# Optimization experiments

Hardware: AMD Instinct MI355X
Metric: run time of the kernel (lower is better)

The kernel has to match this reference:

```python
import jax, jax.numpy as jnp
import numpy as np

EMBED = 1024
N_HEADS = 16
HEAD_DIM = EMBED // N_HEADS
B, T = 2, 2048


def setup_inputs() -> dict:
    key = jax.random.key(0)
    k1, k2, k3 = jax.random.split(key, 3)
    x = jax.random.normal(k1, (B, T, EMBED), dtype=jnp.float32)
    # torch nn.Linear(embed, 3*embed, bias=False): weight [3C, C]; store as [C, 3C] for x @ W
    w_attn = jax.random.normal(k2, (EMBED, 3 * EMBED), dtype=jnp.float32) * (EMBED ** -0.5)
    w_proj = jax.random.normal(k3, (EMBED, EMBED), dtype=jnp.float32) * (EMBED ** -0.5)
    return {"x": x, "w_attn": w_attn, "w_proj": w_proj}


def reference(x, w_attn, w_proj):
    Bb, Tt, C = x.shape
    kqv = x @ w_attn  # [B, T, 3C]
    # NOTE: original code unpacks as k, q, v (k first)
    k, q, v = jnp.split(kqv, 3, axis=2)
    def heads(t):
        return t.reshape(Bb, Tt, N_HEADS, HEAD_DIM).transpose(0, 2, 1, 3)  # [B, H, T, D]
    k, q, v = heads(k), heads(q), heads(v)
    scale = HEAD_DIM ** -0.5
    wei = jnp.einsum("bhqd,bhkd->bhqk", q, k) * scale  # [B, H, T, T]
    mask = jnp.tril(jnp.ones((Tt, Tt), dtype=bool))
    wei = jnp.where(mask[None, None], wei, -jnp.inf)
    wei = jax.nn.softmax(wei, axis=-1)
    y = jnp.einsum("bhqk,bhkd->bhqd", wei, v)  # [B, H, T, D]
    y = y.transpose(0, 2, 1, 3).reshape(Bb, Tt, C)
    return y @ w_proj
```

## Files before the change

kernel.cpp:

```cpp
#include <hip/hip_runtime.h>

typedef unsigned short u16;
typedef unsigned int u32;

typedef __attribute__((ext_vector_type(4))) float f32x4;
typedef __attribute__((ext_vector_type(8))) short s16x8;
typedef __attribute__((ext_vector_type(4))) short s16x4;

__device__ __forceinline__ u16 f2bf(float f) {
    u32 u = __builtin_bit_cast(u32, f);
    u += 0x7fffu + ((u >> 16) & 1u);
    return (u16)(u >> 16);
}

__device__ __forceinline__ u32 pk_bf16(float a, float b) {
    return (u32)f2bf(a) | ((u32)f2bf(b) << 16);
}

__device__ __forceinline__ u32 cvtpk(float a, float b) {
    u32 r;
    asm("v_cvt_pk_bf16_f32 %0, %1, %2" : "=v"(r) : "v"(a), "v"(b));
    return r;
}

#define EXP2(x) exp2f(x)

__device__ __forceinline__ void gload16(const u16* g, u16* l) {
    __builtin_amdgcn_global_load_lds(
        (const __attribute__((address_space(1))) void*)(const void*)g,
        (__attribute__((address_space(3))) void*)(void*)l, 16, 0, 0);
}

__global__ void k_cast(const float* __restrict__ in, u16* __restrict__ out) {
    int i = (blockIdx.x * 256 + threadIdx.x) * 4;
    float4 v = *(const float4*)(in + i);
    uint2 pk;
    pk.x = pk_bf16(v.x, v.y);
    pk.y = pk_bf16(v.z, v.w);
    *(uint2*)(out + i) = pk;
}

__global__ void k_transpose(const float* __restrict__ in, u16* __restrict__ out,
                            int K, int N) {
    __shared__ float tile[32][33];
    int n0 = blockIdx.x * 32, k0 = blockIdx.y * 32;
    int x = threadIdx.x, y = threadIdx.y;
#pragma unroll
    for (int j = 0; j < 32; j += 8)
        tile[y + j][x] = in[(size_t)(k0 + y + j) * N + n0 + x];
    __syncthreads();
#pragma unroll
    for (int j = 0; j < 32; j += 8)
        out[(size_t)(n0 + y + j) * K + k0 + x] = f2bf(tile[x][y + j]);
}

template <int EPI>
__global__ __launch_bounds__(256, 2) void k_gemm(
        const u16* __restrict__ A, const u16* __restrict__ Bt,
        void* __restrict__ Cout, u16* __restrict__ Vt, int N, int K) {
    __shared__ u16 As[128 * 32];
    __shared__ u16 Bs[128 * 32];
    const int nbn = N >> 7;
    const int bm = (int)blockIdx.x / nbn, bn = (int)blockIdx.x % nbn;
    const int tid = threadIdx.x;
    const int wv = tid >> 6, ln = tid & 63;
    const int lg = ln >> 4, lr = ln & 15;
    const int wr = (wv >> 1) << 6, wc = (wv & 1) << 6;

    const u16* gA = A + (size_t)(bm * 128 + wv * 32 + (ln >> 2)) * K + (ln & 3) * 8;
    const u16* gB = Bt + (size_t)(bn * 128 + wv * 32 + (ln >> 2)) * K + (ln & 3) * 8;
    u16* lA = As + wv * 1024;
    u16* lB = Bs + wv * 1024;

    f32x4 acc[4][4] = {};

    for (int k0 = 0; k0 < K; k0 += 32) {
        gload16(gA + k0, lA);
        gload16(gA + k0 + 16 * K, lA + 512);
        gload16(gB + k0, lB);
        gload16(gB + k0 + 16 * K, lB + 512);
        __syncthreads();
        s16x8 af[4], bf[4];
#pragma unroll
        for (int mi = 0; mi < 4; ++mi)
            af[mi] = *(const s16x8*)&As[(wr + mi * 16 + lr) * 32 + lg * 8];
#pragma unroll
        for (int ni = 0; ni < 4; ++ni)
            bf[ni] = *(const s16x8*)&Bs[(wc + ni * 16 + lr) * 32 + lg * 8];
#pragma unroll
        for (int mi = 0; mi < 4; ++mi)
#pragma unroll
            for (int ni = 0; ni < 4; ++ni)
                acc[mi][ni] = __builtin_amdgcn_mfma_f32_16x16x32_bf16(
                        af[mi], bf[ni], acc[mi][ni], 0, 0, 0);
        __syncthreads();
    }

    const int crow0 = bm * 128 + wr + lg * 4;
    const int ccol0 = bn * 128 + wc + lr;
    if (EPI == 0) {
        float* Co = (float*)Cout;
#pragma unroll
        for (int mi = 0; mi < 4; ++mi)
#pragma unroll
            for (int ni = 0; ni < 4; ++ni)
#pragma unroll
                for (int r = 0; r < 4; ++r)
                    Co[(size_t)(crow0 + mi * 16 + r) * N + ccol0 + ni * 16] =
                            acc[mi][ni][r];
    } else {
        if (bn < 16) {
            const float qs = (bn >= 8) ? 0.18033688011112042f : 1.0f;
            u16* Co = (u16*)Cout;
#pragma unroll
            for (int mi = 0; mi < 4; ++mi)
#pragma unroll
                for (int ni = 0; ni < 4; ++ni)
#pragma unroll
                    for (int r = 0; r < 4; ++r)
                        Co[(size_t)(crow0 + mi * 16 + r) * 3072 + ccol0 + ni * 16] =
                                f2bf(acc[mi][ni][r] * qs);
        } else {
#pragma unroll
            for (int mi = 0; mi < 4; ++mi) {
                int row = crow0 + mi * 16;
                int bb = row >> 11, t = row & 2047;
#pragma unroll
                for (int ni = 0; ni < 4; ++ni) {
                    int hd = ccol0 + ni * 16 - 2048;
                    uint2 pk;
                    pk.x = pk_bf16(acc[mi][ni][0], acc[mi][ni][1]);
                    pk.y = pk_bf16(acc[mi][ni][2], acc[mi][ni][3]);
                    *(uint2*)&Vt[(size_t)(bb * 1024 + hd) * 2048 + t] = pk;
                }
            }
        }
    }
}

__global__ __launch_bounds__(256, 4) void k_attn(
        const u16* __restrict__ kqv, const u16* __restrict__ Vt,
        u16* __restrict__ y) {
    const int orig = blockIdx.x;
    const int xcd = orig & 7, slot = orig >> 3;
    const int bh = xcd * 4 + (slot >> 5);
    const int qs = slot & 31;
    const int qt = (qs & 1) ? (31 - (qs >> 1)) : (qs >> 1);
    const int b = bh >> 4, h = bh & 15;
    const int tid = threadIdx.x;
    const int wave = tid >> 6, lane = tid & 63;
    const int lg = lane >> 4, lr = lane & 15;

    __shared__ u16 Ks[2][64 * 64];
    __shared__ u16 Vs[2][64 * 64];
    __shared__ u16 Ps[4][16 * 64];

    const u16* Kg = kqv + (size_t)b * 2048 * 3072 + h * 64;
    const u16* Qg = Kg + 1024;
    const u16* Vg = Vt + (size_t)bh * 64 * 2048;

    const int srow = wave * 16 + (lane >> 3);
    const int cK = (lane & 7) ^ (lane >> 3);
    const u16* kg0 = Kg + (size_t)srow * 3072 + cK * 8;
    const u16* vg0 = Vg + (size_t)srow * 2048 + cK * 8;

    const int nkt = qt + 1;
    const int qbase = qt * 64 + wave * 16;

    const u16* qrp = Qg + (size_t)(qbase + lr) * 3072;
    const s16x8 qf0 = *(const s16x8*)(qrp + lg * 8);
    const s16x8 qf1 = *(const s16x8*)(qrp + 32 + lg * 8);

    s16x8 ones;
#pragma unroll
    for (int i = 0; i < 8; ++i) ones[i] = (short)0x3F80;

    f32x4 o[4] = {};
    f32x4 l4 = {};

    u16* Psw = &Ps[wave][0];
    const int swz = (lr & 7);

#define STAGE(bb, t)                                            \
    {                                                           \
        const u16* kp_ = kg0 + (size_t)(t) * 64 * 3072;         \
        const u16* vp_ = vg0 + (size_t)(t) * 64;                \
        u16* lk_ = &Ks[bb][wave * 1024];                        \
        u16* lv_ = &Vs[bb][wave * 1024];                        \
        gload16(kp_, lk_);                                      \
        gload16(kp_ + 8 * 3072, lk_ + 512);                     \
        gload16(vp_, lv_);                                      \
        gload16(vp_ + 8 * 2048, lv_ + 512);                     \
    }

    STAGE(0, 0);
    asm volatile("s_waitcnt vmcnt(0)\n\ts_barrier" ::: "memory");

    for (int kt = 0; kt < nkt; ++kt) {
        const int cur = kt & 1;
        if (kt + 1 < nkt) STAGE(cur ^ 1, kt + 1);

        f32x4 st[4];
        __builtin_amdgcn_s_setprio(1);
#pragma unroll
        for (int kb = 0; kb < 4; ++kb) {
            const int row = kb * 16 + lr;
            s16x8 kf0 = *(const s16x8*)&Ks[cur][row * 64 + ((lg ^ swz) << 3)];
            s16x8 kf1 = *(const s16x8*)&Ks[cur][row * 64 + (((4 + lg) ^ swz) << 3)];
            f32x4 z = {};
            z = __builtin_amdgcn_mfma_f32_16x16x32_bf16(kf0, qf0, z, 0, 0, 0);
            z = __builtin_amdgcn_mfma_f32_16x16x32_bf16(kf1, qf1, z, 0, 0, 0);
            st[kb] = z;
        }
        __builtin_amdgcn_s_setprio(0);

        if (kt == nkt - 1) {
            const int q_abs = qbase + lr;
            const int kb0 = kt * 64 + lg * 4;
#pragma unroll
            for (int kb = 0; kb < 4; ++kb)
#pragma unroll
                for (int r = 0; r < 4; ++r)
                    st[kb][r] = EXP2((kb0 + kb * 16 + r <= q_abs)
                                         ? st[kb][r] : -3e38f);
        } else {
#pragma unroll
            for (int kb = 0; kb < 4; ++kb)
#pragma unroll
                for (int r = 0; r < 4; ++r) st[kb][r] = EXP2(st[kb][r]);
        }

#pragma unroll
        for (int kb = 0; kb < 4; ++kb) {
            const int sw = (kb * 4 + lg + lr) & 15;
            uint2 w;
            w.x = cvtpk(st[kb][0], st[kb][1]);
            w.y = cvtpk(st[kb][2], st[kb][3]);
            *(uint2*)&Psw[lr * 64 + sw * 4] = w;
        }
        asm volatile("s_waitcnt lgkmcnt(0)" ::: "memory");
        __builtin_amdgcn_sched_barrier(0);

        __builtin_amdgcn_s_setprio(1);
#pragma unroll
        for (int half = 0; half < 2; ++half) {
            const int s0 = (half * 8 + lg * 2 + lr) & 15;
            const int s1 = (half * 8 + lg * 2 + 1 + lr) & 15;
            s16x4 pa = *(const s16x4*)&Psw[lr * 64 + s0 * 4];
            s16x4 pb = *(const s16x4*)&Psw[lr * 64 + s1 * 4];
            s16x8 pf = __builtin_shufflevector(pa, pb, 0, 1, 2, 3, 4, 5, 6, 7);
            l4 = __builtin_amdgcn_mfma_f32_16x16x32_bf16(ones, pf, l4, 0, 0, 0);
#pragma unroll
            for (int dt = 0; dt < 4; ++dt) {
                const int vrow = dt * 16 + lr;
                s16x8 vf = *(const s16x8*)&Vs[cur][vrow * 64 +
                                                   (((half * 4 + lg) ^ swz) << 3)];
                o[dt] = __builtin_amdgcn_mfma_f32_16x16x32_bf16(vf, pf, o[dt], 0, 0, 0);
            }
        }
        __builtin_amdgcn_s_setprio(0);

        asm volatile("s_waitcnt vmcnt(0)\n\ts_barrier" ::: "memory");
    }
#undef STAGE

    const float inv = 1.0f / l4[0];
    u16* yb = y + (size_t)(b * 2048 + qbase + lr) * 1024 + h * 64;
#pragma unroll
    for (int dt = 0; dt < 4; ++dt) {
        uint2 w;
        w.x = cvtpk(o[dt][0] * inv, o[dt][1] * inv);
        w.y = cvtpk(o[dt][2] * inv, o[dt][3] * inv);
        *(uint2*)(yb + dt * 16 + lg * 4) = w;
    }
}

extern "C" void kernel_launch(void* const* d_in, const int* in_sizes, int n_in,
                              void* d_out, int out_size, void* d_ws, size_t ws_size,
                              hipStream_t stream) {
    const float* x = (const float*)d_in[0];
    const float* w_attn = (const float*)d_in[1];
    const float* w_proj = (const float*)d_in[2];
    float* out = (float*)d_out;
    char* ws = (char*)d_ws;

    u16* x_bf = (u16*)(ws);
    u16* wat  = (u16*)(ws + (size_t)(8 << 20));
    u16* wpt  = (u16*)(ws + (size_t)(14 << 20));
    u16* kqv  = (u16*)(ws + (size_t)(16 << 20));
    u16* vt   = (u16*)(ws + (size_t)(40 << 20));
    u16* yb   = (u16*)(ws + (size_t)(48 << 20));

    k_cast<<<4096, 256, 0, stream>>>(x, x_bf);
    k_transpose<<<dim3(96, 32), dim3(32, 8), 0, stream>>>(w_attn, wat, 1024, 3072);
    k_transpose<<<dim3(32, 32), dim3(32, 8), 0, stream>>>(w_proj, wpt, 1024, 1024);
    k_gemm<1><<<32 * 24, 256, 0, stream>>>(x_bf, wat, kqv, vt, 3072, 1024);
    k_attn<<<1024, 256, 0, stream>>>(kqv, vt, yb);
    k_gemm<0><<<32 * 8, 256, 0, stream>>>(yb, wpt, out, nullptr, 1024, 1024);
}
```

Baseline: 201.7 us.

## Split attention KV tiles across two wave groups and pair causal query tiles

The attention kernel now runs 512-thread blocks. Each block handles a pair of query tiles (qt and 31-qt) in two passes, which balances the causal work across blocks. Within a block, two 4-wave groups take alternating K/V tiles with their own double buffers, and their partial outputs and row sums are merged through shared memory before normalisation. The aim is more parallelism per query tile and even load across blocks. In exchange it adds extra barriers, a combine step that rounds one group's partial output to bf16, and more LDS per block, which may lower occupancy. The P-tile swizzle is also changed so each 8-element fragment is read with one load instead of two.

Result: faster. 179.2 us (-11.2%).

```diff
diff --git a/kernel.cpp b/kernel.cpp
--- a/kernel.cpp
+++ b/kernel.cpp
@@ -5,7 +5,6 @@
 
 typedef __attribute__((ext_vector_type(4))) float f32x4;
 typedef __attribute__((ext_vector_type(8))) short s16x8;
-typedef __attribute__((ext_vector_type(4))) short s16x4;
 
 __device__ __forceinline__ u16 f2bf(float f) {
     u32 u = __builtin_bit_cast(u32, f);
@@ -21,6 +20,11 @@
     u32 r;
     asm("v_cvt_pk_bf16_f32 %0, %1, %2" : "=v"(r) : "v"(a), "v"(b));
     return r;
+}
+
+__device__ __forceinline__ float bf2f(u16 h) {
+    u32 u = ((u32)h) << 16;
+    return __builtin_bit_cast(float, u);
 }
 
 #define EXP2(x) exp2f(x)
@@ -138,141 +142,172 @@
     }
 }
 
-__global__ __launch_bounds__(256, 4) void k_attn(
+__global__ __launch_bounds__(512, 4) void k_attn(
         const u16* __restrict__ kqv, const u16* __restrict__ Vt,
         u16* __restrict__ y) {
     const int orig = blockIdx.x;
     const int xcd = orig & 7, slot = orig >> 3;
-    const int bh = xcd * 4 + (slot >> 5);
-    const int qs = slot & 31;
-    const int qt = (qs & 1) ? (31 - (qs >> 1)) : (qs >> 1);
+    const int bh = xcd * 4 + (slot >> 4);
+    const int pr = slot & 15;
     const int b = bh >> 4, h = bh & 15;
     const int tid = threadIdx.x;
-    const int wave = tid >> 6, lane = tid & 63;
+    const int wave = tid >> 6;
+    const int g = wave >> 2;
+    const int wv4 = wave & 3;
+    const int lane = tid & 63;
     const int lg = lane >> 4, lr = lane & 15;
 
-    __shared__ u16 Ks[2][64 * 64];
-    __shared__ u16 Vs[2][64 * 64];
-    __shared__ u16 Ps[4][16 * 64];
+    __shared__ u16 Ks[2][2][64 * 64];
+    __shared__ u16 Vs[2][2][64 * 64];
+    __shared__ u16 Ps[8][16 * 64];
+    u16* comb = &Ps[0][0];
 
     const u16* Kg = kqv + (size_t)b * 2048 * 3072 + h * 64;
     const u16* Qg = Kg + 1024;
     const u16* Vg = Vt + (size_t)bh * 64 * 2048;
 
-    const int srow = wave * 16 + (lane >> 3);
+    const int srow = wv4 * 16 + (lane >> 3);
     const int cK = (lane & 7) ^ (lane >> 3);
     const u16* kg0 = Kg + (size_t)srow * 3072 + cK * 8;
     const u16* vg0 = Vg + (size_t)srow * 2048 + cK * 8;
-
-    const int nkt = qt + 1;
-    const int qbase = qt * 64 + wave * 16;
-
-    const u16* qrp = Qg + (size_t)(qbase + lr) * 3072;
-    const s16x8 qf0 = *(const s16x8*)(qrp + lg * 8);
-    const s16x8 qf1 = *(const s16x8*)(qrp + 32 + lg * 8);
+    const int swz = lr & 7;
 
     s16x8 ones;
 #pragma unroll
     for (int i = 0; i < 8; ++i) ones[i] = (short)0x3F80;
 
-    f32x4 o[4] = {};
-    f32x4 l4 = {};
-
     u16* Psw = &Ps[wave][0];
-    const int swz = (lr & 7);
-
-#define STAGE(bb, t)                                            \
-    {                                                           \
-        const u16* kp_ = kg0 + (size_t)(t) * 64 * 3072;         \
-        const u16* vp_ = vg0 + (size_t)(t) * 64;                \
-        u16* lk_ = &Ks[bb][wave * 1024];                        \
-        u16* lv_ = &Vs[bb][wave * 1024];                        \
-        gload16(kp_, lk_);                                      \
-        gload16(kp_ + 8 * 3072, lk_ + 512);                     \
-        gload16(vp_, lv_);                                      \
-        gload16(vp_ + 8 * 2048, lv_ + 512);                     \
+
+#define STAGE(bb, t)                                      \
+    {                                                     \
+        const u16* kp_ = kg0 + (size_t)(t) * 64 * 3072;   \
+        const u16* vp_ = vg0 + (size_t)(t) * 64;          \
+        u16* lk_ = &Ks[g][bb][wv4 * 1024];                \
+        u16* lv_ = &Vs[g][bb][wv4 * 1024];                \
+        gload16(kp_, lk_);                                \
+        gload16(kp_ + 8 * 3072, lk_ + 512);               \
+        gload16(vp_, lv_);                                \
+        gload16(vp_ + 8 * 2048, lv_ + 512);               \
     }
 
-    STAGE(0, 0);
-    asm volatile("s_waitcnt vmcnt(0)\n\ts_barrier" ::: "memory");
-
-    for (int kt = 0; kt < nkt; ++kt) {
-        const int cur = kt & 1;
-        if (kt + 1 < nkt) STAGE(cur ^ 1, kt + 1);
-
-        f32x4 st[4];
-        __builtin_amdgcn_s_setprio(1);
-#pragma unroll
-        for (int kb = 0; kb < 4; ++kb) {
-            const int row = kb * 16 + lr;
-            s16x8 kf0 = *(const s16x8*)&Ks[cur][row * 64 + ((lg ^ swz) << 3)];
-            s16x8 kf1 = *(const s16x8*)&Ks[cur][row * 64 + (((4 + lg) ^ swz) << 3)];
-            f32x4 z = {};
-            z = __builtin_amdgcn_mfma_f32_16x16x32_bf16(kf0, qf0, z, 0, 0, 0);
-            z = __builtin_amdgcn_mfma_f32_16x16x32_bf16(kf1, qf1, z, 0, 0, 0);
-            st[kb] = z;
+    for (int pass = 0; pass < 2; ++pass) {
+        const int qt = pass ? (31 - pr) : pr;
+        const int nkt = qt + 1;
+        const int iters = (nkt + 1) >> 1;
+        const int qbase = qt * 64 + wv4 * 16;
+
+        const u16* qrp = Qg + (size_t)(qbase + lr) * 3072;
+        const s16x8 qf0 = *(const s16x8*)(qrp + lg * 8);
+        const s16x8 qf1 = *(const s16x8*)(qrp + 32 + lg * 8);
+
+        f32x4 o[4] = {};
+        f32x4 l4 = {};
+
+        if (g < nkt) STAGE(0, g);
+        asm volatile("s_waitcnt vmcnt(0)\n\ts_barrier" ::: "memory");
+
+        for (int i = 0; i < iters; ++i) {
+            const int cur = i & 1;
+            const int t = 2 * i + g;
+            if (t + 2 < nkt) STAGE(cur ^ 1, t + 2);
+            if (t < nkt) {
+                f32x4 st[4];
+                __builtin_amdgcn_s_setprio(1);
+#pragma unroll
+                for (int kb = 0; kb < 4; ++kb) {
+                    const int row = kb * 16 + lr;
+                    s16x8 kf0 = *(const s16x8*)&Ks[g][cur][row * 64 + ((lg ^ swz) << 3)];
+                    s16x8 kf1 = *(const s16x8*)&Ks[g][cur][row * 64 + (((4 + lg) ^ swz) << 3)];
+                    f32x4 z = {};
+                    z = __builtin_amdgcn_mfma_f32_16x16x32_bf16(kf0, qf0, z, 0, 0, 0);
+                    z = __builtin_amdgcn_mfma_f32_16x16x32_bf16(kf1, qf1, z, 0, 0, 0);
+                    st[kb] = z;
+                }
+                __builtin_amdgcn_s_setprio(0);
+
+                if (t == nkt - 1) {
+                    const int q_abs = qbase + lr;
+                    const int kb0 = t * 64 + lg * 4;
+#pragma unroll
+                    for (int kb = 0; kb < 4; ++kb)
+#pragma unroll
+                        for (int r = 0; r < 4; ++r)
+                            st[kb][r] = EXP2((kb0 + kb * 16 + r <= q_abs)
+                                                 ? st[kb][r] : -3e38f);
+                } else {
+#pragma unroll
+                    for (int kb = 0; kb < 4; ++kb)
+#pragma unroll
+                        for (int r = 0; r < 4; ++r) st[kb][r] = EXP2(st[kb][r]);
+                }
+
+#pragma unroll
+                for (int kb = 0; kb < 4; ++kb) {
+                    const int kbs = (kb + lr) & 3;
+                    uint2 w;
+                    w.x = cvtpk(st[kb][0], st[kb][1]);
+                    w.y = cvtpk(st[kb][2], st[kb][3]);
+                    *(uint2*)&Psw[lr * 64 + kbs * 16 + lg * 4] = w;
+                }
+                asm volatile("s_waitcnt lgkmcnt(0)" ::: "memory");
+                __builtin_amdgcn_sched_barrier(0);
+
+                __builtin_amdgcn_s_setprio(1);
+#pragma unroll
+                for (int half = 0; half < 2; ++half) {
+                    const int kbs = ((half * 2 + (lg >> 1)) + lr) & 3;
+                    s16x8 pf = *(const s16x8*)&Psw[lr * 64 + kbs * 16 + (lg & 1) * 8];
+                    l4 = __builtin_amdgcn_mfma_f32_16x16x32_bf16(ones, pf, l4, 0, 0, 0);
+#pragma unroll
+                    for (int dt = 0; dt < 4; ++dt) {
+                        const int vrow = dt * 16 + lr;
+                        s16x8 vf = *(const s16x8*)&Vs[g][cur][vrow * 64 +
+                                                    (((half * 4 + lg) ^ swz) << 3)];
+                        o[dt] = __builtin_amdgcn_mfma_f32_16x16x32_bf16(vf, pf, o[dt], 0, 0, 0);
+                    }
+                }
+                __builtin_amdgcn_s_setprio(0);
+            }
+            asm volatile("s_waitcnt vmcnt(0)\n\ts_barrier" ::: "memory");
         }
-        __builtin_amdgcn_s_setprio(0);
-
-        if (kt == nkt - 1) {
-            const int q_abs = qbase + lr;
-            const int kb0 = kt * 64 + lg * 4;
-#pragma unroll
-            for (int kb = 0; kb < 4; ++kb)
-#pragma unroll
-                for (int r = 0; r < 4; ++r)
-                    st[kb][r] = EXP2((kb0 + kb * 16 + r <= q_abs)
-                                         ? st[kb][r] : -3e38f);
-        } else {
-#pragma unroll
-            for (int kb = 0; kb < 4; ++kb)
-#pragma unroll
-                for (int r = 0; r < 4; ++r) st[kb][r] = EXP2(st[kb][r]);
+
+        __syncthreads();
+        if (g == 1) {
+            u16* ce = comb + (size_t)(wv4 * 64 + lane) * 20;
+#pragma unroll
+            for (int dt = 0; dt < 4; ++dt) {
+                uint2 w;
+                w.x = cvtpk(o[dt][0], o[dt][1]);
+                w.y = cvtpk(o[dt][2], o[dt][3]);
+                *(uint2*)(ce + dt * 4) = w;
+            }
+            *(float*)(ce + 16) = l4[0];
         }
-
-#pragma unroll
-        for (int kb = 0; kb < 4; ++kb) {
-            const int sw = (kb * 4 + lg + lr) & 15;
-            uint2 w;
-            w.x = cvtpk(st[kb][0], st[kb][1]);
-            w.y = cvtpk(st[kb][2], st[kb][3]);
-            *(uint2*)&Psw[lr * 64 + sw * 4] = w;
+        __syncthreads();
+        if (g == 0) {
+            const u16* ce = comb + (size_t)(wv4 * 64 + lane) * 20;
+            float l = l4[0] + *(const float*)(ce + 16);
+#pragma unroll
+            for (int dt = 0; dt < 4; ++dt) {
+                uint2 w = *(const uint2*)(ce + dt * 4);
+                o[dt][0] += bf2f((u16)(w.x & 0xffff));
+                o[dt][1] += bf2f((u16)(w.x >> 16));
+                o[dt][2] += bf2f((u16)(w.y & 0xffff));
+                o[dt][3] += bf2f((u16)(w.y >> 16));
+            }
+            const float inv = 1.0f / l;
+            u16* yb = y + (size_t)(b * 2048 + qbase + lr) * 1024 + h * 64;
+#pragma unroll
+            for (int dt = 0; dt < 4; ++dt) {
+                uint2 w;
+                w.x = cvtpk(o[dt][0] * inv, o[dt][1] * inv);
+                w.y = cvtpk(o[dt][2] * inv, o[dt][3] * inv);
+                *(uint2*)(yb + dt * 16 + lg * 4) = w;
+            }
         }
-        asm volatile("s_waitcnt lgkmcnt(0)" ::: "memory");
-        __builtin_amdgcn_sched_barrier(0);
-
-        __builtin_amdgcn_s_setprio(1);
-#pragma unroll
-        for (int half = 0; half < 2; ++half) {
-            const int s0 = (half * 8 + lg * 2 + lr) & 15;
-            const int s1 = (half * 8 + lg * 2 + 1 + lr) & 15;
-            s16x4 pa = *(const s16x4*)&Psw[lr * 64 + s0 * 4];
-            s16x4 pb = *(const s16x4*)&Psw[lr * 64 + s1 * 4];
-            s16x8 pf = __builtin_shufflevector(pa, pb, 0, 1, 2, 3, 4, 5, 6, 7);
-            l4 = __builtin_amdgcn_mfma_f32_16x16x32_bf16(ones, pf, l4, 0, 0, 0);
-#pragma unroll
-            for (int dt = 0; dt < 4; ++dt) {
-                const int vrow = dt * 16 + lr;
-                s16x8 vf = *(const s16x8*)&Vs[cur][vrow * 64 +
-                                                   (((half * 4 + lg) ^ swz) << 3)];
-                o[dt] = __builtin_amdgcn_mfma_f32_16x16x32_bf16(vf, pf, o[dt], 0, 0, 0);
-            }
-        }
-        __builtin_amdgcn_s_setprio(0);
-
-        asm volatile("s_waitcnt vmcnt(0)\n\ts_barrier" ::: "memory");
+        __syncthreads();
     }
 #undef STAGE
-
-    const float inv = 1.0f / l4[0];
-    u16* yb = y + (size_t)(b * 2048 + qbase + lr) * 1024 + h * 64;
-#pragma unroll
-    for (int dt = 0; dt < 4; ++dt) {
-        uint2 w;
-        w.x = cvtpk(o[dt][0] * inv, o[dt][1] * inv);
-        w.y = cvtpk(o[dt][2] * inv, o[dt][3] * inv);
-        *(uint2*)(yb + dt * 16 + lg * 4) = w;
-    }
 }
 
 extern "C" void kernel_launch(void* const* d_in, const int* in_sizes, int n_in,
@@ -295,6 +330,6 @@
     k_transpose<<<dim3(96, 32), dim3(32, 8), 0, stream>>>(w_attn, wat, 1024, 3072);
     k_transpose<<<dim3(32, 32), dim3(32, 8), 0, stream>>>(w_proj, wpt, 1024, 1024);
     k_gemm<1><<<32 * 24, 256, 0, stream>>>(x_bf, wat, kqv, vt, 3072, 1024);
-    k_attn<<<1024, 256, 0, stream>>>(kqv, vt, yb);
+    k_attn<<<512, 512, 0, stream>>>(kqv, vt, yb);
     k_gemm<0><<<32 * 8, 256, 0, stream>>>(yb, wpt, out, nullptr, 1024, 1024);
 }
```
